# Optimization experiments

Measured on AMD Instinct MI355X. Metric: run time of the kernel, lower is better.

The kernel has to match this reference:

```python
import jax, jax.numpy as jnp
import numpy as np

TAIL = 10.0
K = 8
MIN_W = 1e-3
MIN_H = 1e-3
MIN_D = 1e-3
EPS = 1e-12
D_ID = 32   # identity dims
D_TR = 32   # transformed dims
HID = 256


def setup_inputs() -> dict:
    key = jax.random.key(0)
    k0, k1, k2, k3, k4 = jax.random.split(key, 5)
    B = 131072
    inputs = jax.random.normal(k0, (B, D_ID + D_TR), dtype=jnp.float32)
    W1 = jax.random.normal(k1, (D_ID, HID), dtype=jnp.float32) * (1.0 / np.sqrt(D_ID))
    b1 = jnp.zeros((HID,), dtype=jnp.float32)
    W2 = jax.random.normal(k2, (HID, D_TR * (3 * K + 1)), dtype=jnp.float32) * (1.0 / np.sqrt(HID))
    b2 = jnp.zeros((D_TR * (3 * K + 1),), dtype=jnp.float32)
    return {"inputs": inputs, "W1": W1, "b1": b1, "W2": W2, "b2": b2}


def _normalize_bin_params(un_w, un_h, un_d):
    # widths
    w = jax.nn.softmax(un_w, axis=-1)
    w = MIN_W + (1.0 - MIN_W * K) * w
    cw = jnp.cumsum(w, axis=-1)
    cw = jnp.pad(cw, [(0, 0)] * (cw.ndim - 1) + [(1, 0)])
    cw = cw / jnp.clip(cw[..., -1:], 1e-12)
    w = cw[..., 1:] - cw[..., :-1]
    # heights
    h = jax.nn.softmax(un_h, axis=-1)
    h = MIN_H + (1.0 - MIN_H * K) * h
    ch = jnp.cumsum(h, axis=-1)
    ch = jnp.pad(ch, [(0, 0)] * (ch.ndim - 1) + [(1, 0)])
    ch = ch / jnp.clip(ch[..., -1:], 1e-12)
    h = ch[..., 1:] - ch[..., :-1]
    d = MIN_D + jax.nn.softplus(un_d)
    return w, cw, h, ch, d


def _rqs_forward(x, w, cw, h, ch, d):
    # x: (N,); bins: (N,K) / (N,K+1). Linear tails outside [-TAIL, TAIL].
    inside = (x >= -TAIL) & (x <= TAIL)
    xs = jnp.clip((x + TAIL) / (2.0 * TAIL), 0.0, 1.0)
    bin_ids = jnp.clip(jnp.sum(xs[:, None] >= cw, axis=-1) - 1, 0, K - 1)
    take = lambda t, idx: jnp.take_along_axis(t, idx[:, None], axis=-1)[:, 0]
    xk = take(cw, bin_ids)
    wk = take(w, bin_ids)
    yk = take(ch, bin_ids)
    hk = take(h, bin_ids)
    dk = take(d, bin_ids)
    dk1 = take(d, bin_ids + 1)
    t = jnp.clip((xs - xk) / (wk + EPS), 0.0, 1.0)
    a = (hk + EPS) / (wk + EPS)
    b = dk
    c = dk1
    num = a * t * t + b * t * (1.0 - t)
    den = a + (b + c - 2.0 * a) * t * (1.0 - t)
    s = num / (den + EPS)
    ys = yk + hk * s
    y = ys * (2.0 * TAIL) - TAIL
    deriv_num = a * a * (c * t * t + 2.0 * a * t * (1.0 - t) + b * (1.0 - t) * (1.0 - t))
    dydx = deriv_num / (den * den + EPS)  # (top-bottom)/(right-left) == 1
    lad = jnp.log(jnp.clip(dydx, 1e-12))
    return jnp.where(inside, y, x), jnp.where(inside, lad, 0.0)


def reference(inputs, W1, b1, W2, b2):
    identity = inputs[:, :D_ID]          # mask <= 0 columns
    to_transform = inputs[:, D_ID:]      # mask > 0 columns
    Bsz = inputs.shape[0]
    params = jax.nn.relu(identity @ W1 + b1) @ W2 + b2
    p = params.reshape(Bsz, D_TR, 3 * K + 1)
    un_w, un_h, un_d = p[..., :K], p[..., K:2 * K], p[..., 2 * K:]
    w, cw, h, ch, d = _normalize_bin_params(un_w, un_h, un_d)
    # flatten (Bsz, D_TR, ...) -> (Bsz*D_TR, ...)
    xf = to_transform.reshape(-1)
    yf, ladf = _rqs_forward(
        xf,
        w.reshape(-1, K), cw.reshape(-1, K + 1),
        h.reshape(-1, K), ch.reshape(-1, K + 1),
        d.reshape(-1, K + 1),
    )
    outputs = jnp.concatenate([identity, yf.reshape(Bsz, D_TR)], axis=1)
    logabsdet = ladf.reshape(Bsz, D_TR).sum(axis=1)
    return outputs, logabsdet
```

## Files before the change

### kernel.cpp

```cpp
#include <hip/hip_runtime.h>
#include <math.h>

#define NROWS 131072
#define HID 256
#define NPAR 800
#define MROWS 32
#define NTHREADS 512
#define NBLOCKS (NROWS / MROWS)

#define W2F_FRAGS 25600
#define LDS_HLO 16384
#define LDS_X   32768
#define LDS_PLD 804
#define LDS_TOTAL (16 * LDS_PLD * 4)

typedef __attribute__((ext_vector_type(8))) short s16x8;
typedef __attribute__((ext_vector_type(4))) float f32x4;

__device__ __forceinline__ unsigned short bf16_rne(float f) {
    unsigned u = __float_as_uint(f);
    u += 0x7fffu + ((u >> 16) & 1u);
    return (unsigned short)(u >> 16);
}

__global__ void prep_w2(const float* __restrict__ W2, short* __restrict__ wsp)
{
    const int t = blockIdx.x * 256 + threadIdx.x;
    if (t >= W2F_FRAGS) return;
    const int l = t & 63;
    const int g = t >> 6;
    const int ct = g >> 3, k0 = g & 7;
    const int c  = (ct << 4) + (l & 15);
    const int kb = (k0 << 5) + ((l >> 4) << 3);
    s16x8 hi, lo;
#pragma unroll
    for (int j = 0; j < 8; ++j) {
        float v = W2[(size_t)(kb + j) * NPAR + c];
        unsigned short h = bf16_rne(v);
        float hf = __uint_as_float((unsigned)h << 16);
        unsigned short lw = bf16_rne(v - hf);
        hi[j] = (short)h;
        lo[j] = (short)lw;
    }
    ((s16x8*)wsp)[g * 128 + l * 2]     = hi;
    ((s16x8*)wsp)[g * 128 + l * 2 + 1] = lo;
}

__global__ __launch_bounds__(NTHREADS, 4)
void rqs_fused(const float* __restrict__ inp,
               const float* __restrict__ W1,
               const float* __restrict__ b1,
               const short* __restrict__ W2F,
               const float* __restrict__ b2,
               float* __restrict__ out)
{
    extern __shared__ char smem[];
    char*  hhi   = smem;
    char*  hlo   = smem + LDS_HLO;
    float* x_lds = (float*)(smem + LDS_X);
    float* p_lds = (float*)smem;

    const int t    = threadIdx.x;
    const int row0 = blockIdx.x * MROWS;
    const int lane = t & 63;
    const int w    = t >> 6;
    const int arow = lane & 15;
    const int kgrp = lane >> 4;
    const int lane2 = lane << 1;

    const s16x8* BF = (const s16x8*)W2F;

    const int nct = (w < 2) ? 7 : 6;

    if (t < 256) {
        const int r = t >> 3, q = t & 7;
        const float4 v = ((const float4*)(inp + (size_t)(row0 + r) * 64))[q];
        ((float4*)(out + (size_t)(row0 + r) * 64))[q] = v;
        ((float4*)(x_lds + r * 32))[q] = v;
    }
    __syncthreads();

    {
        const int j = t & 255;
        const int q = t >> 8;
        float w1v[32];
#pragma unroll
        for (int k = 0; k < 32; ++k) w1v[k] = W1[k * HID + j];
        const float bj = b1[j];
        for (int rr = 0; rr < 16; ++rr) {
            const int r = q * 16 + rr;
            const float4* xr = (const float4*)(x_lds + r * 32);
            float s0 = bj, s1 = 0.f, s2 = 0.f, s3 = 0.f;
#pragma unroll
            for (int qq = 0; qq < 8; ++qq) {
                const float4 xv = xr[qq];
                s0 = fmaf(xv.x, w1v[4 * qq + 0], s0);
                s1 = fmaf(xv.y, w1v[4 * qq + 1], s1);
                s2 = fmaf(xv.z, w1v[4 * qq + 2], s2);
                s3 = fmaf(xv.w, w1v[4 * qq + 3], s3);
            }
            const float s = fmaxf((s0 + s1) + (s2 + s3), 0.0f);
            unsigned short hs = bf16_rne(s);
            float hf = __uint_as_float((unsigned)hs << 16);
            unsigned short ls = bf16_rne(s - hf);
            int byte = (r << 9) + (j << 1);
            byte ^= (r & 7) << 4;
            *(short*)(hhi + byte) = (short)hs;
            *(short*)(hlo + byte) = (short)ls;
        }
    }
    __syncthreads();

    f32x4 acc[7][2];
#pragma unroll
    for (int ci = 0; ci < 7; ++ci) {
        acc[ci][0] = (f32x4){0.f, 0.f, 0.f, 0.f};
        acc[ci][1] = (f32x4){0.f, 0.f, 0.f, 0.f};
    }

#pragma unroll 1
    for (int k0 = 0; k0 < 8; ++k0) {
        s16x8 ahi[2], alo[2];
#pragma unroll
        for (int rt = 0; rt < 2; ++rt) {
            const int row = rt * 16 + arow;
            int byte = (row << 9) + (k0 << 6) + (kgrp << 4);
            byte ^= (row & 7) << 4;
            ahi[rt] = *(const s16x8*)(hhi + byte);
            alo[rt] = *(const s16x8*)(hlo + byte);
        }
#pragma unroll
        for (int ci = 0; ci < 7; ++ci) {
            if (ci < nct) {
                const int ct = w + (ci << 3);
                const int f  = (ct * 8 + k0) * 128 + lane2;
                const s16x8 bh = BF[f];
                const s16x8 bl = BF[f + 1];
                __builtin_amdgcn_s_setprio(1);
                acc[ci][0] = __builtin_amdgcn_mfma_f32_16x16x32_bf16(ahi[0], bh, acc[ci][0], 0, 0, 0);
                acc[ci][1] = __builtin_amdgcn_mfma_f32_16x16x32_bf16(ahi[1], bh, acc[ci][1], 0, 0, 0);
                acc[ci][0] = __builtin_amdgcn_mfma_f32_16x16x32_bf16(ahi[0], bl, acc[ci][0], 0, 0, 0);
                acc[ci][1] = __builtin_amdgcn_mfma_f32_16x16x32_bf16(ahi[1], bl, acc[ci][1], 0, 0, 0);
                acc[ci][0] = __builtin_amdgcn_mfma_f32_16x16x32_bf16(alo[0], bh, acc[ci][0], 0, 0, 0);
                acc[ci][1] = __builtin_amdgcn_mfma_f32_16x16x32_bf16(alo[1], bh, acc[ci][1], 0, 0, 0);
                __builtin_amdgcn_s_setprio(0);
            }
        }
    }

#pragma unroll
    for (int rhalf = 0; rhalf < 2; ++rhalf) {
        __syncthreads();
#pragma unroll
        for (int ci = 0; ci < 7; ++ci) {
            if (ci < nct) {
                const int ct = w + (ci << 3);
                const float bias = b2[(ct << 4) + arow];
                const int col = (ct << 4) + arow;
                const f32x4 v = acc[ci][rhalf];
                const int rowl = kgrp << 2;
                p_lds[(rowl + 0) * LDS_PLD + col] = v[0] + bias;
                p_lds[(rowl + 1) * LDS_PLD + col] = v[1] + bias;
                p_lds[(rowl + 2) * LDS_PLD + col] = v[2] + bias;
                p_lds[(rowl + 3) * LDS_PLD + col] = v[3] + bias;
            }
        }
        __syncthreads();

        {
            const int r_l = t >> 5;
            const int dl  = t & 31;
            const float* p = &p_lds[r_l * LDS_PLD + dl * 25];
            float pv[25];
#pragma unroll
            for (int j = 0; j < 25; ++j) pv[j] = p[j];

            float cw[9], ch[9], dd[9];
            {
                float mw = pv[0];
#pragma unroll
                for (int j = 1; j < 8; ++j) mw = fmaxf(mw, pv[j]);
                float e[8], sw = 0.f;
#pragma unroll
                for (int j = 0; j < 8; ++j) { e[j] = __expf(pv[j] - mw); sw += e[j]; }
                const float scale = 0.992f / sw;
                float run = 0.f;
                cw[0] = 0.f;
#pragma unroll
                for (int j = 0; j < 8; ++j) { run += 0.001f + e[j] * scale; cw[j + 1] = run; }
                const float icn = 1.0f / fmaxf(cw[8], 1e-12f);
#pragma unroll
                for (int j = 1; j <= 8; ++j) cw[j] *= icn;
            }
            {
                float mh = pv[8];
#pragma unroll
                for (int j = 1; j < 8; ++j) mh = fmaxf(mh, pv[8 + j]);
                float e[8], sh = 0.f;
#pragma unroll
                for (int j = 0; j < 8; ++j) { e[j] = __expf(pv[8 + j] - mh); sh += e[j]; }
                const float scale = 0.992f / sh;
                float run = 0.f;
                ch[0] = 0.f;
#pragma unroll
                for (int j = 0; j < 8; ++j) { run += 0.001f + e[j] * scale; ch[j + 1] = run; }
                const float icn = 1.0f / fmaxf(ch[8], 1e-12f);
#pragma unroll
                for (int j = 1; j <= 8; ++j) ch[j] *= icn;
            }
#pragma unroll
            for (int j = 0; j < 9; ++j) {
                const float u = pv[16 + j];
                dd[j] = 0.001f + fmaxf(u, 0.f) + __logf(1.0f + __expf(-fabsf(u)));
            }

            const int grow = row0 + rhalf * 16 + r_l;
            const float x = inp[(size_t)grow * 64 + 32 + dl];
            const float xs = fminf(fmaxf((x + 10.0f) * 0.05f, 0.f), 1.f);
            int b = 0;
#pragma unroll
            for (int j = 1; j <= 8; ++j) b += (xs >= cw[j]) ? 1 : 0;
            b = min(b, 7);

            float xk = 0.f, wk = 0.f, yk = 0.f, hk = 0.f, dk = 0.f, dk1 = 0.f;
#pragma unroll
            for (int j = 0; j < 8; ++j) {
                if (b == j) {
                    xk = cw[j]; wk = cw[j + 1] - cw[j];
                    yk = ch[j]; hk = ch[j + 1] - ch[j];
                    dk = dd[j]; dk1 = dd[j + 1];
                }
            }

            const float EPSf = 1e-12f;
            const float tt = fminf(fmaxf((xs - xk) / (wk + EPSf), 0.f), 1.f);
            const float a = (hk + EPSf) / (wk + EPSf);
            const float omt = 1.f - tt;
            const float tomt = tt * omt;
            const float num = a * tt * tt + dk * tomt;
            const float den = a + (dk + dk1 - 2.f * a) * tomt;
            const float sres = num / (den + EPSf);
            const float ys = yk + hk * sres;
            float y = ys * 20.0f - 10.0f;
            const float dnum = a * a * (dk1 * tt * tt + 2.f * a * tomt + dk * omt * omt);
            const float dydx = dnum / (den * den + EPSf);
            float lad = __logf(fmaxf(dydx, 1e-12f));

            const bool inside = (x >= -10.0f) && (x <= 10.0f);
            if (!inside) { y = x; lad = 0.0f; }

            out[(size_t)grow * 64 + 32 + dl] = y;

            float s = lad;
            s += __shfl_xor(s, 1, 64);
            s += __shfl_xor(s, 2, 64);
            s += __shfl_xor(s, 4, 64);
            s += __shfl_xor(s, 8, 64);
            s += __shfl_xor(s, 16, 64);
            if ((lane & 31) == 0) out[(size_t)NROWS * 64 + grow] = s;
        }
    }
}

extern "C" void kernel_launch(void* const* d_in, const int* in_sizes, int n_in,
                              void* d_out, int out_size, void* d_ws, size_t ws_size,
                              hipStream_t stream) {
    const float* inp = (const float*)d_in[0];
    const float* W1  = (const float*)d_in[1];
    const float* b1  = (const float*)d_in[2];
    const float* W2  = (const float*)d_in[3];
    const float* b2  = (const float*)d_in[4];
    float* out = (float*)d_out;
    short* wsp = (short*)d_ws;

    hipLaunchKernelGGL(prep_w2, dim3(100), dim3(256), 0, stream, W2, wsp);
    hipLaunchKernelGGL(rqs_fused, dim3(NBLOCKS), dim3(NTHREADS), LDS_TOTAL, stream,
                       inp, W1, b1, (const short*)wsp, b2, out);
}
```

Before: 297.7 us.

## Compute first layer with split-bf16 MFMA and evaluate softplus only for selected bins

The first dense layer (inputs×W1) moves off per-thread FP32 FMA loops and onto bf16 MFMA instructions. W1 and the input rows are each split into hi and lo bf16 parts to keep near-FP32 accuracy, and W1's fragments are pre-packed by the prep kernel. The input tile in LDS gets an XOR swizzle to match the new fragment loads. Softplus for the derivative parameters is now computed only for the two selected knots instead of all nine, which saves transcendental work but adds a select chain.

```diff
diff --git a/kernel.cpp b/kernel.cpp
--- a/kernel.cpp
+++ b/kernel.cpp
@@ -9,6 +9,7 @@
 #define NBLOCKS (NROWS / MROWS)
 
 #define W2F_FRAGS 25600
+#define W1F_BASE  51200
 #define LDS_HLO 16384
 #define LDS_X   32768
 #define LDS_PLD 804
@@ -22,33 +23,53 @@
     u += 0x7fffu + ((u >> 16) & 1u);
     return (unsigned short)(u >> 16);
 }
-
-__global__ void prep_w2(const float* __restrict__ W2, short* __restrict__ wsp)
+__device__ __forceinline__ float bf16_to_f(unsigned short h) {
+    return __uint_as_float((unsigned)h << 16);
+}
+
+__global__ void prep_w(const float* __restrict__ W2, const float* __restrict__ W1,
+                       short* __restrict__ wsp)
 {
     const int t = blockIdx.x * 256 + threadIdx.x;
-    if (t >= W2F_FRAGS) return;
-    const int l = t & 63;
-    const int g = t >> 6;
-    const int ct = g >> 3, k0 = g & 7;
-    const int c  = (ct << 4) + (l & 15);
-    const int kb = (k0 << 5) + ((l >> 4) << 3);
-    s16x8 hi, lo;
-#pragma unroll
-    for (int j = 0; j < 8; ++j) {
-        float v = W2[(size_t)(kb + j) * NPAR + c];
-        unsigned short h = bf16_rne(v);
-        float hf = __uint_as_float((unsigned)h << 16);
-        unsigned short lw = bf16_rne(v - hf);
-        hi[j] = (short)h;
-        lo[j] = (short)lw;
-    }
-    ((s16x8*)wsp)[g * 128 + l * 2]     = hi;
-    ((s16x8*)wsp)[g * 128 + l * 2 + 1] = lo;
+    if (t < W2F_FRAGS) {
+        const int l = t & 63;
+        const int g = t >> 6;
+        const int ct = g >> 3, k0 = g & 7;
+        const int c  = (ct << 4) + (l & 15);
+        const int kb = (k0 << 5) + ((l >> 4) << 3);
+        s16x8 hi, lo;
+#pragma unroll
+        for (int j = 0; j < 8; ++j) {
+            float v = W2[(size_t)(kb + j) * NPAR + c];
+            unsigned short h = bf16_rne(v);
+            unsigned short lw = bf16_rne(v - bf16_to_f(h));
+            hi[j] = (short)h;
+            lo[j] = (short)lw;
+        }
+        ((s16x8*)wsp)[g * 128 + l * 2]     = hi;
+        ((s16x8*)wsp)[g * 128 + l * 2 + 1] = lo;
+    } else if (t < W2F_FRAGS + 1024) {
+        const int t1 = t - W2F_FRAGS;
+        const int l  = t1 & 63;
+        const int ct = t1 >> 6;
+        const int c  = (ct << 4) + (l & 15);
+        const int kb = (l >> 4) << 3;
+        s16x8 hi, lo;
+#pragma unroll
+        for (int j = 0; j < 8; ++j) {
+            float v = W1[(size_t)(kb + j) * HID + c];
+            unsigned short h = bf16_rne(v);
+            unsigned short lw = bf16_rne(v - bf16_to_f(h));
+            hi[j] = (short)h;
+            lo[j] = (short)lw;
+        }
+        ((s16x8*)wsp)[W1F_BASE + ct * 128 + l * 2]     = hi;
+        ((s16x8*)wsp)[W1F_BASE + ct * 128 + l * 2 + 1] = lo;
+    }
 }
 
 __global__ __launch_bounds__(NTHREADS, 4)
 void rqs_fused(const float* __restrict__ inp,
-               const float* __restrict__ W1,
                const float* __restrict__ b1,
                const short* __restrict__ W2F,
                const float* __restrict__ b2,
@@ -57,7 +78,7 @@
     extern __shared__ char smem[];
     char*  hhi   = smem;
     char*  hlo   = smem + LDS_HLO;
-    float* x_lds = (float*)(smem + LDS_X);
+    char*  x_c   = smem + LDS_X;
     float* p_lds = (float*)smem;
 
     const int t    = threadIdx.x;
@@ -76,37 +97,70 @@
         const int r = t >> 3, q = t & 7;
         const float4 v = ((const float4*)(inp + (size_t)(row0 + r) * 64))[q];
         ((float4*)(out + (size_t)(row0 + r) * 64))[q] = v;
-        ((float4*)(x_lds + r * 32))[q] = v;
+        int byte = (r << 7) + (q << 4);
+        byte ^= (r & 7) << 4;
+        *(float4*)(x_c + byte) = v;
     }
     __syncthreads();
 
     {
-        const int j = t & 255;
-        const int q = t >> 8;
-        float w1v[32];
-#pragma unroll
-        for (int k = 0; k < 32; ++k) w1v[k] = W1[k * HID + j];
-        const float bj = b1[j];
-        for (int rr = 0; rr < 16; ++rr) {
-            const int r = q * 16 + rr;
-            const float4* xr = (const float4*)(x_lds + r * 32);
-            float s0 = bj, s1 = 0.f, s2 = 0.f, s3 = 0.f;
-#pragma unroll
-            for (int qq = 0; qq < 8; ++qq) {
-                const float4 xv = xr[qq];
-                s0 = fmaf(xv.x, w1v[4 * qq + 0], s0);
-                s1 = fmaf(xv.y, w1v[4 * qq + 1], s1);
-                s2 = fmaf(xv.z, w1v[4 * qq + 2], s2);
-                s3 = fmaf(xv.w, w1v[4 * qq + 3], s3);
-            }
-            const float s = fmaxf((s0 + s1) + (s2 + s3), 0.0f);
-            unsigned short hs = bf16_rne(s);
-            float hf = __uint_as_float((unsigned)hs << 16);
-            unsigned short ls = bf16_rne(s - hf);
-            int byte = (r << 9) + (j << 1);
-            byte ^= (r & 7) << 4;
-            *(short*)(hhi + byte) = (short)hs;
-            *(short*)(hlo + byte) = (short)ls;
+        const int c0 = (2 * w) * 128 + W1F_BASE + lane2;
+        const int c1 = (2 * w + 1) * 128 + W1F_BASE + lane2;
+        const s16x8 w1h0 = BF[c0], w1l0 = BF[c0 + 1];
+        const s16x8 w1h1 = BF[c1], w1l1 = BF[c1 + 1];
+
+        s16x8 xhi[2], xlo[2];
+#pragma unroll
+        for (int rt = 0; rt < 2; ++rt) {
+            const int row  = rt * 16 + arow;
+            const int base = (row << 7) + (kgrp << 5);
+            const int sw   = (row & 7) << 4;
+            const float4 va = *(const float4*)(x_c + (base ^ sw));
+            const float4 vb = *(const float4*)(x_c + ((base + 16) ^ sw));
+            const float xv[8] = {va.x, va.y, va.z, va.w, vb.x, vb.y, vb.z, vb.w};
+#pragma unroll
+            for (int j = 0; j < 8; ++j) {
+                unsigned short h = bf16_rne(xv[j]);
+                xhi[rt][j] = (short)h;
+                xlo[rt][j] = (short)bf16_rne(xv[j] - bf16_to_f(h));
+            }
+        }
+
+        const float bias0 = b1[(2 * w) * 16 + arow];
+        const float bias1 = b1[(2 * w + 1) * 16 + arow];
+        f32x4 g[2][2];
+        g[0][0] = (f32x4){bias0, bias0, bias0, bias0};
+        g[1][0] = (f32x4){bias0, bias0, bias0, bias0};
+        g[0][1] = (f32x4){bias1, bias1, bias1, bias1};
+        g[1][1] = (f32x4){bias1, bias1, bias1, bias1};
+
+#pragma unroll
+        for (int rt = 0; rt < 2; ++rt) {
+            g[rt][0] = __builtin_amdgcn_mfma_f32_16x16x32_bf16(xhi[rt], w1h0, g[rt][0], 0, 0, 0);
+            g[rt][1] = __builtin_amdgcn_mfma_f32_16x16x32_bf16(xhi[rt], w1h1, g[rt][1], 0, 0, 0);
+            g[rt][0] = __builtin_amdgcn_mfma_f32_16x16x32_bf16(xhi[rt], w1l0, g[rt][0], 0, 0, 0);
+            g[rt][1] = __builtin_amdgcn_mfma_f32_16x16x32_bf16(xhi[rt], w1l1, g[rt][1], 0, 0, 0);
+            g[rt][0] = __builtin_amdgcn_mfma_f32_16x16x32_bf16(xlo[rt], w1h0, g[rt][0], 0, 0, 0);
+            g[rt][1] = __builtin_amdgcn_mfma_f32_16x16x32_bf16(xlo[rt], w1h1, g[rt][1], 0, 0, 0);
+        }
+
+#pragma unroll
+        for (int rt = 0; rt < 2; ++rt) {
+#pragma unroll
+            for (int ci = 0; ci < 2; ++ci) {
+                const int col = (2 * w + ci) * 16 + arow;
+#pragma unroll
+                for (int i = 0; i < 4; ++i) {
+                    const int row = rt * 16 + (kgrp << 2) + i;
+                    const float s = fmaxf(g[rt][ci][i], 0.0f);
+                    unsigned short hs = bf16_rne(s);
+                    unsigned short ls = bf16_rne(s - bf16_to_f(hs));
+                    int byte = (row << 9) + (col << 1);
+                    byte ^= (row & 7) << 4;
+                    *(short*)(hhi + byte) = (short)hs;
+                    *(short*)(hlo + byte) = (short)ls;
+                }
+            }
         }
     }
     __syncthreads();
@@ -175,7 +229,7 @@
 #pragma unroll
             for (int j = 0; j < 25; ++j) pv[j] = p[j];
 
-            float cw[9], ch[9], dd[9];
+            float cw[9], ch[9];
             {
                 float mw = pv[0];
 #pragma unroll
@@ -208,11 +262,6 @@
 #pragma unroll
                 for (int j = 1; j <= 8; ++j) ch[j] *= icn;
             }
-#pragma unroll
-            for (int j = 0; j < 9; ++j) {
-                const float u = pv[16 + j];
-                dd[j] = 0.001f + fmaxf(u, 0.f) + __logf(1.0f + __expf(-fabsf(u)));
-            }
 
             const int grow = row0 + rhalf * 16 + r_l;
             const float x = inp[(size_t)grow * 64 + 32 + dl];
@@ -222,15 +271,23 @@
             for (int j = 1; j <= 8; ++j) b += (xs >= cw[j]) ? 1 : 0;
             b = min(b, 7);
 
-            float xk = 0.f, wk = 0.f, yk = 0.f, hk = 0.f, dk = 0.f, dk1 = 0.f;
+            float xk = 0.f, wk = 0.f, yk = 0.f, hk = 0.f;
 #pragma unroll
             for (int j = 0; j < 8; ++j) {
                 if (b == j) {
                     xk = cw[j]; wk = cw[j + 1] - cw[j];
                     yk = ch[j]; hk = ch[j + 1] - ch[j];
-                    dk = dd[j]; dk1 = dd[j + 1];
                 }
             }
+            float ud0 = pv[16], ud1 = pv[17];
+#pragma unroll
+            for (int j = 1; j < 8; ++j) {
+                const bool ge = (b >= j);
+                ud0 = ge ? pv[16 + j] : ud0;
+                ud1 = ge ? pv[17 + j] : ud1;
+            }
+            const float dk  = 0.001f + fmaxf(ud0, 0.f) + __logf(1.0f + __expf(-fabsf(ud0)));
+            const float dk1 = 0.001f + fmaxf(ud1, 0.f) + __logf(1.0f + __expf(-fabsf(ud1)));
 
             const float EPSf = 1e-12f;
             const float tt = fminf(fmaxf((xs - xk) / (wk + EPSf), 0.f), 1.f);
@@ -273,7 +330,7 @@
     float* out = (float*)d_out;
     short* wsp = (short*)d_ws;
 
-    hipLaunchKernelGGL(prep_w2, dim3(100), dim3(256), 0, stream, W2, wsp);
+    hipLaunchKernelGGL(prep_w, dim3(104), dim3(256), 0, stream, W2, W1, wsp);
     hipLaunchKernelGGL(rqs_fused, dim3(NBLOCKS), dim3(NTHREADS), LDS_TOTAL, stream,
-                       inp, W1, b1, (const short*)wsp, b2, out);
-}
+                       inp, b1, (const short*)wsp, b2, out);
+}
```

Measured after the change: 268.5 us. -9.8%, faster.
